# Kernel optimization log

Measured on AMD Instinct MI355X. Metric: run time of the kernel, lower is better.

## Reference

```python
import jax, jax.numpy as jnp
import numpy as np

TEMP = 0.1
EPS = 1e-12  # torch F.normalize eps


def _normalize(v):
    return v / jnp.maximum(jnp.linalg.norm(v, axis=1, keepdims=True), EPS)


def _scale_loss(a1, a2, b1, c1):
    # diag of exp(a1 @ a2.T / temp): computed directly from paired rows
    # (same math as eye-mask + row-sum in the original).
    diag = jnp.exp(jnp.sum(a1 * a2, axis=1) / TEMP)            # [B]
    denom = (jnp.exp(a1 @ b1.T / TEMP).sum(1, keepdims=True)
             + jnp.exp(a1 @ c1.T / TEMP).sum(1, keepdims=True))  # [B,1]
    # NOTE: [B] / [B,1] broadcasts to [B,B], exactly as in the torch code.
    return jnp.mean(-jnp.log(diag / denom))


def setup_inputs() -> dict:
    key = jax.random.key(0)
    kx, ky, kz = jax.random.split(key, 3)
    shape = (8192, 128)
    return {
        "x": jax.random.normal(kx, shape, dtype=jnp.float32),
        "y": jax.random.normal(ky, shape, dtype=jnp.float32),
        "z": jax.random.normal(kz, shape, dtype=jnp.float32),
    }


def reference(x, y, z):
    x = _normalize(x)
    y = _normalize(y)
    z = _normalize(z)
    B = x.shape[0] // 2
    x1, x2 = x[:B], x[B:]
    y1, y2 = y[:B], y[B:]
    z1, z2 = z[:B], z[B:]

    loss_scale = (_scale_loss(x1, x2, y1, z1)
                  + _scale_loss(y1, y2, x1, z1)
                  + _scale_loss(z1, z2, x1, y1))

    xyz1 = jnp.concatenate([x1, y1, z1], axis=1)  # [B, 3D]
    xyz2 = jnp.concatenate([x2, y2, z2], axis=1)
    m = jnp.exp(xyz1 @ xyz2.T / TEMP)             # [B, B]
    # [B] / [B,1] -> [B,B] broadcast, matching the torch code.
    loss_view = jnp.mean(-jnp.log(jnp.diagonal(m) / m.sum(1, keepdims=True)))

    return loss_view + loss_scale
```

## Files before the change

kernel.cpp:

```cpp
#include <hip/hip_runtime.h>
#include <hip/hip_bf16.h>

#define BHALF 4096
#define DDIM 128
#define KCAT 384
#define TEMP_INV 10.0f

typedef __attribute__((ext_vector_type(8))) short short8;
typedef __attribute__((ext_vector_type(4))) float f32x4;

__global__ __launch_bounds__(256) void normalize_kernel(
    const float* __restrict__ x, const float* __restrict__ y,
    const float* __restrict__ z,
    ushort* __restrict__ nrm1, ushort* __restrict__ nrm2) {
  int wave = threadIdx.x >> 6;
  int lane = threadIdx.x & 63;
  int gr = blockIdx.x * 4 + wave;
  int mat = gr >> 13;
  int r = gr & 8191;
  const float* src = (mat == 0 ? x : (mat == 1 ? y : z)) + (size_t)r * DDIM;
  float2 v = *(const float2*)(src + lane * 2);
  float s = v.x * v.x + v.y * v.y;
#pragma unroll
  for (int m = 1; m < 64; m <<= 1) s += __shfl_xor(s, m, 64);
  float scale = 1.0f / fmaxf(sqrtf(s), 1e-12f);
  ushort* dst = (r < BHALF ? nrm1 + (size_t)r * KCAT
                           : nrm2 + (size_t)(r - BHALF) * KCAT)
                + mat * DDIM + lane * 2;
  __hip_bfloat162 o;
  o.x = __float2bfloat16(v.x * scale);
  o.y = __float2bfloat16(v.y * scale);
  *(__hip_bfloat162*)dst = o;
}

__global__ __launch_bounds__(256) void diag_kernel(
    const float* __restrict__ x, const float* __restrict__ y,
    const float* __restrict__ z, float* __restrict__ dxyz) {
  int wave = threadIdx.x >> 6;
  int lane = threadIdx.x & 63;
  int i = blockIdx.x * 4 + wave;
  const float* mats[3] = {x, y, z};
#pragma unroll
  for (int m = 0; m < 3; ++m) {
    const float* p1 = mats[m] + (size_t)i * DDIM;
    const float* p2 = mats[m] + (size_t)(i + BHALF) * DDIM;
    float2 a = *(const float2*)(p1 + lane * 2);
    float2 b = *(const float2*)(p2 + lane * 2);
    float s1 = a.x * a.x + a.y * a.y;
    float s2 = b.x * b.x + b.y * b.y;
    float d = a.x * b.x + a.y * b.y;
#pragma unroll
    for (int mm = 1; mm < 64; mm <<= 1) {
      s1 += __shfl_xor(s1, mm, 64);
      s2 += __shfl_xor(s2, mm, 64);
      d += __shfl_xor(d, mm, 64);
    }
    if (lane == 0)
      dxyz[m * BHALF + i] =
          d / (fmaxf(sqrtf(s1), 1e-12f) * fmaxf(sqrtf(s2), 1e-12f));
  }
}

__global__ __launch_bounds__(256) void gram_kernel(
    const ushort* __restrict__ nrm1, const ushort* __restrict__ nrm2,
    float* __restrict__ sums) {
  int g = blockIdx.z;
  const ushort* Abase;
  const ushort* Bbase;
  int K;
  float* rs;
  float* cs;
  if (g == 0) {
    Abase = nrm1; Bbase = nrm1 + 128; K = 128;
    rs = sums; cs = sums + 4096;
  } else if (g == 1) {
    Abase = nrm1; Bbase = nrm1 + 256; K = 128;
    rs = sums + 2 * 4096; cs = sums + 3 * 4096;
  } else if (g == 2) {
    Abase = nrm1 + 128; Bbase = nrm1 + 256; K = 128;
    rs = sums + 4 * 4096; cs = sums + 5 * 4096;
  } else {
    Abase = nrm1; Bbase = nrm2; K = 384;
    rs = sums + 6 * 4096; cs = nullptr;
  }

  __shared__ ushort As[128][40];
  __shared__ ushort Bs[128][40];

  int tid = threadIdx.x;
  int lane = tid & 63;
  int wave = tid >> 6;
  int wr = wave >> 1;
  int wc = wave & 1;

  int rowbase = blockIdx.x * 128;
  int colbase = blockIdx.y * 128;

  f32x4 acc[4][4] = {};

  for (int k0 = 0; k0 < K; k0 += 32) {
    __syncthreads();
#pragma unroll
    for (int it = 0; it < 2; ++it) {
      int idx = tid + it * 256;
      int row = idx >> 2;
      int chunk = idx & 3;
      *(uint4*)&As[row][chunk * 8] =
          *(const uint4*)(Abase + (size_t)(rowbase + row) * KCAT + k0 + chunk * 8);
      *(uint4*)&Bs[row][chunk * 8] =
          *(const uint4*)(Bbase + (size_t)(colbase + row) * KCAT + k0 + chunk * 8);
    }
    __syncthreads();
    short8 af[4], bf[4];
    int rsel = lane & 15;
    int ksel = (lane >> 4) * 8;
#pragma unroll
    for (int m = 0; m < 4; ++m)
      af[m] = *(const short8*)&As[wr * 64 + m * 16 + rsel][ksel];
#pragma unroll
    for (int n = 0; n < 4; ++n)
      bf[n] = *(const short8*)&Bs[wc * 64 + n * 16 + rsel][ksel];
#pragma unroll
    for (int m = 0; m < 4; ++m)
#pragma unroll
      for (int n = 0; n < 4; ++n)
        acc[m][n] = __builtin_amdgcn_mfma_f32_16x16x32_bf16(af[m], bf[n],
                                                            acc[m][n], 0, 0, 0);
  }

#pragma unroll
  for (int m = 0; m < 4; ++m)
#pragma unroll
    for (int n = 0; n < 4; ++n)
#pragma unroll
      for (int r = 0; r < 4; ++r)
        acc[m][n][r] = __expf(acc[m][n][r] * TEMP_INV);

#pragma unroll
  for (int m = 0; m < 4; ++m) {
    float rsum[4];
#pragma unroll
    for (int r = 0; r < 4; ++r)
      rsum[r] = acc[m][0][r] + acc[m][1][r] + acc[m][2][r] + acc[m][3][r];
#pragma unroll
    for (int r = 0; r < 4; ++r) {
      rsum[r] += __shfl_xor(rsum[r], 1, 64);
      rsum[r] += __shfl_xor(rsum[r], 2, 64);
      rsum[r] += __shfl_xor(rsum[r], 4, 64);
      rsum[r] += __shfl_xor(rsum[r], 8, 64);
    }
    if ((lane & 15) == 0) {
      int rbase = rowbase + wr * 64 + m * 16 + (lane >> 4) * 4;
#pragma unroll
      for (int r = 0; r < 4; ++r) atomicAdd(&rs[rbase + r], rsum[r]);
    }
  }

  if (cs != nullptr) {
#pragma unroll
    for (int n = 0; n < 4; ++n) {
      float csum = 0.0f;
#pragma unroll
      for (int m = 0; m < 4; ++m)
#pragma unroll
        for (int r = 0; r < 4; ++r) csum += acc[m][n][r];
      csum += __shfl_xor(csum, 16, 64);
      csum += __shfl_xor(csum, 32, 64);
      if (lane < 16) atomicAdd(&cs[colbase + wc * 64 + n * 16 + lane], csum);
    }
  }
}

__global__ __launch_bounds__(256) void loss_kernel(
    const float* __restrict__ sums, const float* __restrict__ dxyz,
    float* __restrict__ out) {
  const float* rs0 = sums;
  const float* cs0 = sums + 4096;
  const float* rs1 = sums + 2 * 4096;
  const float* cs1 = sums + 3 * 4096;
  const float* rs2 = sums + 4 * 4096;
  const float* cs2 = sums + 5 * 4096;
  const float* rs3 = sums + 6 * 4096;
  const float* dx = dxyz;
  const float* dy = dxyz + 4096;
  const float* dz = dxyz + 2 * 4096;
  float acc = 0.0f;
  for (int i = threadIdx.x; i < BHALF; i += 256) {
    float lx = logf(rs0[i] + rs1[i]) - TEMP_INV * dx[i];
    float ly = logf(cs0[i] + rs2[i]) - TEMP_INV * dy[i];
    float lz = logf(cs1[i] + cs2[i]) - TEMP_INV * dz[i];
    float lv = logf(rs3[i]) - TEMP_INV * (dx[i] + dy[i] + dz[i]);
    acc += lx + ly + lz + lv;
  }
  __shared__ float red[4];
#pragma unroll
  for (int m = 1; m < 64; m <<= 1) acc += __shfl_xor(acc, m, 64);
  if ((threadIdx.x & 63) == 0) red[threadIdx.x >> 6] = acc;
  __syncthreads();
  if (threadIdx.x == 0)
    out[0] = (red[0] + red[1] + red[2] + red[3]) * (1.0f / 4096.0f);
}

extern "C" void kernel_launch(void* const* d_in, const int* in_sizes, int n_in,
                              void* d_out, int out_size, void* d_ws,
                              size_t ws_size, hipStream_t stream) {
  const float* x = (const float*)d_in[0];
  const float* y = (const float*)d_in[1];
  const float* z = (const float*)d_in[2];
  char* ws = (char*)d_ws;
  ushort* nrm1 = (ushort*)ws;
  ushort* nrm2 = nrm1 + (size_t)BHALF * KCAT;
  float* sums = (float*)(ws + 2 * (size_t)BHALF * KCAT * sizeof(ushort));
  float* dxyz = sums + 7 * 4096;

  hipMemsetAsync(sums, 0, 7 * 4096 * sizeof(float), stream);
  normalize_kernel<<<3 * 8192 / 4, 256, 0, stream>>>(x, y, z, nrm1, nrm2);
  diag_kernel<<<BHALF / 4, 256, 0, stream>>>(x, y, z, dxyz);
  gram_kernel<<<dim3(32, 32, 4), 256, 0, stream>>>(nrm1, nrm2, sums);
  loss_kernel<<<1, 256, 0, stream>>>(sums, dxyz, (float*)d_out);
}
```

Before: 88.59 us.

## Fuse normalize and diag kernels, use direct global-to-LDS loads with swizzle in gram

Merges the normalize and diagonal kernels into one pass that reads each paired row once and derives the diagonal from the fp32 norms. The gram kernel now fills LDS with global_load_lds (16-byte direct loads) into an XOR-swizzled unpadded layout instead of staging through registers. The loss kernel is widened to 1024 threads. This removes a launch and redundant input reads and cuts register traffic in the GEMM load path, at the cost of a second barrier per k-step and reliance on the swizzle being bank-conflict-free.

```diff
diff --git a/kernel.cpp b/kernel.cpp
--- a/kernel.cpp
+++ b/kernel.cpp
@@ -9,56 +9,45 @@
 typedef __attribute__((ext_vector_type(8))) short short8;
 typedef __attribute__((ext_vector_type(4))) float f32x4;
 
-__global__ __launch_bounds__(256) void normalize_kernel(
+__device__ __forceinline__ void gload16(const ushort* g, ushort* l) {
+  __builtin_amdgcn_global_load_lds(
+      (const __attribute__((address_space(1))) unsigned int*)g,
+      (__attribute__((address_space(3))) unsigned int*)l, 16, 0, 0);
+}
+
+__global__ __launch_bounds__(256) void norm_diag_kernel(
     const float* __restrict__ x, const float* __restrict__ y,
-    const float* __restrict__ z,
-    ushort* __restrict__ nrm1, ushort* __restrict__ nrm2) {
+    const float* __restrict__ z, ushort* __restrict__ nrm1,
+    ushort* __restrict__ nrm2, float* __restrict__ dxyz) {
   int wave = threadIdx.x >> 6;
   int lane = threadIdx.x & 63;
-  int gr = blockIdx.x * 4 + wave;
-  int mat = gr >> 13;
-  int r = gr & 8191;
-  const float* src = (mat == 0 ? x : (mat == 1 ? y : z)) + (size_t)r * DDIM;
-  float2 v = *(const float2*)(src + lane * 2);
-  float s = v.x * v.x + v.y * v.y;
-#pragma unroll
-  for (int m = 1; m < 64; m <<= 1) s += __shfl_xor(s, m, 64);
-  float scale = 1.0f / fmaxf(sqrtf(s), 1e-12f);
-  ushort* dst = (r < BHALF ? nrm1 + (size_t)r * KCAT
-                           : nrm2 + (size_t)(r - BHALF) * KCAT)
-                + mat * DDIM + lane * 2;
-  __hip_bfloat162 o;
-  o.x = __float2bfloat16(v.x * scale);
-  o.y = __float2bfloat16(v.y * scale);
-  *(__hip_bfloat162*)dst = o;
-}
-
-__global__ __launch_bounds__(256) void diag_kernel(
-    const float* __restrict__ x, const float* __restrict__ y,
-    const float* __restrict__ z, float* __restrict__ dxyz) {
-  int wave = threadIdx.x >> 6;
-  int lane = threadIdx.x & 63;
-  int i = blockIdx.x * 4 + wave;
-  const float* mats[3] = {x, y, z};
-#pragma unroll
-  for (int m = 0; m < 3; ++m) {
-    const float* p1 = mats[m] + (size_t)i * DDIM;
-    const float* p2 = mats[m] + (size_t)(i + BHALF) * DDIM;
-    float2 a = *(const float2*)(p1 + lane * 2);
-    float2 b = *(const float2*)(p2 + lane * 2);
-    float s1 = a.x * a.x + a.y * a.y;
-    float s2 = b.x * b.x + b.y * b.y;
-    float d = a.x * b.x + a.y * b.y;
-#pragma unroll
-    for (int mm = 1; mm < 64; mm <<= 1) {
-      s1 += __shfl_xor(s1, mm, 64);
-      s2 += __shfl_xor(s2, mm, 64);
-      d += __shfl_xor(d, mm, 64);
-    }
-    if (lane == 0)
-      dxyz[m * BHALF + i] =
-          d / (fmaxf(sqrtf(s1), 1e-12f) * fmaxf(sqrtf(s2), 1e-12f));
-  }
+  int gi = blockIdx.x * 4 + wave;
+  int mat = gi >> 12;
+  int i = gi & 4095;
+  const float* src = (mat == 0 ? x : (mat == 1 ? y : z));
+  float2 a = *(const float2*)(src + (size_t)i * DDIM + lane * 2);
+  float2 b = *(const float2*)(src + (size_t)(i + BHALF) * DDIM + lane * 2);
+  float s1 = a.x * a.x + a.y * a.y;
+  float s2 = b.x * b.x + b.y * b.y;
+  float d = a.x * b.x + a.y * b.y;
+#pragma unroll
+  for (int m = 1; m < 64; m <<= 1) {
+    s1 += __shfl_xor(s1, m, 64);
+    s2 += __shfl_xor(s2, m, 64);
+    d += __shfl_xor(d, m, 64);
+  }
+  float r1 = 1.0f / fmaxf(sqrtf(s1), 1e-12f);
+  float r2 = 1.0f / fmaxf(sqrtf(s2), 1e-12f);
+  ushort* d1 = nrm1 + (size_t)i * KCAT + mat * DDIM + lane * 2;
+  ushort* d2 = nrm2 + (size_t)i * KCAT + mat * DDIM + lane * 2;
+  __hip_bfloat162 o1, o2;
+  o1.x = __float2bfloat16(a.x * r1);
+  o1.y = __float2bfloat16(a.y * r1);
+  o2.x = __float2bfloat16(b.x * r2);
+  o2.y = __float2bfloat16(b.y * r2);
+  *(__hip_bfloat162*)d1 = o1;
+  *(__hip_bfloat162*)d2 = o2;
+  if (lane == 0) dxyz[mat * BHALF + i] = d * r1 * r2;
 }
 
 __global__ __launch_bounds__(256) void gram_kernel(
@@ -84,8 +73,8 @@
     rs = sums + 6 * 4096; cs = nullptr;
   }
 
-  __shared__ ushort As[128][40];
-  __shared__ ushort Bs[128][40];
+  __shared__ ushort As[128][32];
+  __shared__ ushort Bs[128][32];
 
   int tid = threadIdx.x;
   int lane = tid & 63;
@@ -96,36 +85,46 @@
   int rowbase = blockIdx.x * 128;
   int colbase = blockIdx.y * 128;
 
+  int lrow = lane >> 2;
+  int lchunk8 = (((lane & 3) ^ ((lrow >> 1) & 3)) << 3);
+  const ushort* gA0 =
+      Abase + (size_t)(rowbase + wave * 16 + lrow) * KCAT + lchunk8;
+  const ushort* gA1 = gA0 + (size_t)64 * KCAT;
+  const ushort* gB0 =
+      Bbase + (size_t)(colbase + wave * 16 + lrow) * KCAT + lchunk8;
+  const ushort* gB1 = gB0 + (size_t)64 * KCAT;
+  ushort* lA0 = &As[wave * 16][0];
+  ushort* lA1 = &As[wave * 16 + 64][0];
+  ushort* lB0 = &Bs[wave * 16][0];
+  ushort* lB1 = &Bs[wave * 16 + 64][0];
+
+  int rsel = lane & 15;
+  int slot8 = (((lane >> 4) ^ ((rsel >> 1) & 3)) << 3);
+
   f32x4 acc[4][4] = {};
 
-  for (int k0 = 0; k0 < K; k0 += 32) {
-    __syncthreads();
-#pragma unroll
-    for (int it = 0; it < 2; ++it) {
-      int idx = tid + it * 256;
-      int row = idx >> 2;
-      int chunk = idx & 3;
-      *(uint4*)&As[row][chunk * 8] =
-          *(const uint4*)(Abase + (size_t)(rowbase + row) * KCAT + k0 + chunk * 8);
-      *(uint4*)&Bs[row][chunk * 8] =
-          *(const uint4*)(Bbase + (size_t)(colbase + row) * KCAT + k0 + chunk * 8);
-    }
+  int ksteps = K >> 5;
+  for (int ks = 0; ks < ksteps; ++ks) {
+    gload16(gA0, lA0);
+    gload16(gA1, lA1);
+    gload16(gB0, lB0);
+    gload16(gB1, lB1);
+    gA0 += 32; gA1 += 32; gB0 += 32; gB1 += 32;
     __syncthreads();
     short8 af[4], bf[4];
-    int rsel = lane & 15;
-    int ksel = (lane >> 4) * 8;
 #pragma unroll
     for (int m = 0; m < 4; ++m)
-      af[m] = *(const short8*)&As[wr * 64 + m * 16 + rsel][ksel];
+      af[m] = *(const short8*)&As[wr * 64 + m * 16 + rsel][slot8];
 #pragma unroll
     for (int n = 0; n < 4; ++n)
-      bf[n] = *(const short8*)&Bs[wc * 64 + n * 16 + rsel][ksel];
+      bf[n] = *(const short8*)&Bs[wc * 64 + n * 16 + rsel][slot8];
 #pragma unroll
     for (int m = 0; m < 4; ++m)
 #pragma unroll
       for (int n = 0; n < 4; ++n)
         acc[m][n] = __builtin_amdgcn_mfma_f32_16x16x32_bf16(af[m], bf[n],
                                                             acc[m][n], 0, 0, 0);
+    __syncthreads();
   }
 
 #pragma unroll
@@ -171,7 +170,7 @@
   }
 }
 
-__global__ __launch_bounds__(256) void loss_kernel(
+__global__ __launch_bounds__(1024) void loss_kernel(
     const float* __restrict__ sums, const float* __restrict__ dxyz,
     float* __restrict__ out) {
   const float* rs0 = sums;
@@ -181,24 +180,29 @@
   const float* rs2 = sums + 4 * 4096;
   const float* cs2 = sums + 5 * 4096;
   const float* rs3 = sums + 6 * 4096;
-  const float* dx = dxyz;
-  const float* dy = dxyz + 4096;
-  const float* dz = dxyz + 2 * 4096;
+  int tid = threadIdx.x;
   float acc = 0.0f;
-  for (int i = threadIdx.x; i < BHALF; i += 256) {
-    float lx = logf(rs0[i] + rs1[i]) - TEMP_INV * dx[i];
-    float ly = logf(cs0[i] + rs2[i]) - TEMP_INV * dy[i];
-    float lz = logf(cs1[i] + cs2[i]) - TEMP_INV * dz[i];
-    float lv = logf(rs3[i]) - TEMP_INV * (dx[i] + dy[i] + dz[i]);
+  for (int i = tid; i < BHALF; i += 1024) {
+    float dxv = dxyz[i];
+    float dyv = dxyz[4096 + i];
+    float dzv = dxyz[2 * 4096 + i];
+    float lx = logf(rs0[i] + rs1[i]) - TEMP_INV * dxv;
+    float ly = logf(cs0[i] + rs2[i]) - TEMP_INV * dyv;
+    float lz = logf(cs1[i] + cs2[i]) - TEMP_INV * dzv;
+    float lv = logf(rs3[i]) - TEMP_INV * (dxv + dyv + dzv);
     acc += lx + ly + lz + lv;
   }
-  __shared__ float red[4];
+  __shared__ float red[16];
 #pragma unroll
   for (int m = 1; m < 64; m <<= 1) acc += __shfl_xor(acc, m, 64);
-  if ((threadIdx.x & 63) == 0) red[threadIdx.x >> 6] = acc;
+  if ((tid & 63) == 0) red[tid >> 6] = acc;
   __syncthreads();
-  if (threadIdx.x == 0)
-    out[0] = (red[0] + red[1] + red[2] + red[3]) * (1.0f / 4096.0f);
+  if (tid == 0) {
+    float t = 0.0f;
+#pragma unroll
+    for (int i = 0; i < 16; ++i) t += red[i];
+    out[0] = t * (1.0f / 4096.0f);
+  }
 }
 
 extern "C" void kernel_launch(void* const* d_in, const int* in_sizes, int n_in,
@@ -214,8 +218,8 @@
   float* dxyz = sums + 7 * 4096;
 
   hipMemsetAsync(sums, 0, 7 * 4096 * sizeof(float), stream);
-  normalize_kernel<<<3 * 8192 / 4, 256, 0, stream>>>(x, y, z, nrm1, nrm2);
-  diag_kernel<<<BHALF / 4, 256, 0, stream>>>(x, y, z, dxyz);
+  norm_diag_kernel<<<3 * BHALF / 4, 256, 0, stream>>>(x, y, z, nrm1, nrm2,
+                                                      dxyz);
   gram_kernel<<<dim3(32, 32, 4), 256, 0, stream>>>(nrm1, nrm2, sums);
-  loss_kernel<<<1, 256, 0, stream>>>(sums, dxyz, (float*)d_out);
-}
+  loss_kernel<<<1, 1024, 0, stream>>>(sums, dxyz, (float*)d_out);
+}
```

New measurement: 77.47 us. 1.14x faster.
